# Optimization experiments

Measured on AMD Instinct MI355X. Metric: run time of the kernel, lower is better.

The kernel has to match this reference:

```python
import jax, jax.numpy as jnp
import numpy as np
import math

B, N, C = 8, 4096, 768
H = 12
DH = C // H
M = 256
LN_EPS = 1e-5


def setup_inputs() -> dict:
    key = jax.random.key(0)
    ks = jax.random.split(key, 7)
    x = jax.random.normal(ks[0], (B, N, C), dtype=jnp.float32)
    # torch Linear weight [out,in]; store transposed for y = x @ W
    W_qkv = jax.random.normal(ks[1], (C, 3 * C), dtype=jnp.float32) * (1.0 / math.sqrt(C))
    W_proj = jax.random.normal(ks[2], (C, C), dtype=jnp.float32) * (1.0 / math.sqrt(C))
    b_proj = jnp.zeros((C,), dtype=jnp.float32)
    gamma = jnp.ones((C,), dtype=jnp.float32)
    beta = jnp.zeros((C,), dtype=jnp.float32)
    random_features = jax.random.normal(ks[3], (M, DH), dtype=jnp.float32) / math.sqrt(DH)
    return {"x": x, "W_qkv": W_qkv, "W_proj": W_proj, "b_proj": b_proj,
            "gamma": gamma, "beta": beta, "random_features": random_features}


def _phi(t, random_features):
    # t: [B, H, N, DH] -> [B, H, N, M]; phi(x) = exp(w·x - ||x||^2/2) / sqrt(M)
    norm_sq = 0.5 * jnp.sum(t * t, axis=-1, keepdims=True)
    proj = jnp.einsum('bhnd,md->bhnm', t, random_features)
    return jnp.exp(proj - norm_sq) * (1.0 / math.sqrt(M))


def reference(x, W_qkv, W_proj, b_proj, gamma, beta, random_features):
    b, n, c = x.shape
    qkv = (x @ W_qkv).reshape(b, n, 3, H, DH)
    qkv = jnp.transpose(qkv, (2, 0, 3, 1, 4))  # [3, B, H, N, DH]
    q, k, v = qkv[0], qkv[1], qkv[2]

    q_p = _phi(q, random_features)  # [B,H,N,M]
    k_p = _phi(k, random_features)  # [B,H,N,M]

    kv = jnp.einsum('bhnm,bhnd->bhmd', k_p, v)       # [B,H,M,DH]
    out = jnp.einsum('bhnm,bhmd->bhnd', q_p, kv)     # [B,H,N,DH]

    k_sum = jnp.sum(k_p, axis=2)                      # [B,H,M]
    normalizer = jnp.einsum('bhnm,bhm->bhn', q_p, k_sum)[..., None]
    out = out / (normalizer + 1e-6)

    x_attn = jnp.transpose(out, (0, 2, 1, 3)).reshape(b, n, c)
    x_attn = x_attn @ W_proj + b_proj
    # dropout is identity in eval / p=0

    y = x + x_attn
    mu = jnp.mean(y, axis=-1, keepdims=True)
    var = jnp.mean(jnp.square(y - mu), axis=-1, keepdims=True)
    return (y - mu) * jax.lax.rsqrt(var + LN_EPS) * gamma + beta
```

## Files before the change

### kernel.cpp

```cpp
#include <hip/hip_runtime.h>
#include <hip/hip_fp16.h>


#define LOG2E 1.44269504088896340736f

typedef _Float16 half8 __attribute__((ext_vector_type(8)));
typedef _Float16 half4_t __attribute__((ext_vector_type(4)));
typedef _Float16 half2_t __attribute__((ext_vector_type(2)));
typedef float f32x4 __attribute__((ext_vector_type(4)));

#if __has_builtin(__builtin_amdgcn_fdot2)
#define FDOT2(a, b, c) __builtin_amdgcn_fdot2((a), (b), (c), false)
#else
#define FDOT2(a, b, c) \
  ((float)(a)[0] * (float)(b)[0] + ((float)(a)[1] * (float)(b)[1] + (c)))
#endif

static __device__ __forceinline__ half2_t pk2(float a, float b) {
#if __has_builtin(__builtin_amdgcn_cvt_pkrtz)
  return __builtin_bit_cast(half2_t, __builtin_amdgcn_cvt_pkrtz(a, b));
#else
  half2_t r; r[0] = (_Float16)a; r[1] = (_Float16)b; return r;
#endif
}

__device__ __forceinline__ void glds16(const _Float16* g, _Float16* s) {
  __builtin_amdgcn_global_load_lds(
      (const __attribute__((address_space(1))) void*)g,
      (__attribute__((address_space(3))) unsigned int*)s,
      16, 0, 0);
}


__global__ __launch_bounds__(256)
void prep(const float* __restrict__ x, const float* __restrict__ Wqkv,
          const float* __restrict__ Wproj, const float* __restrict__ rfm,
          _Float16* __restrict__ x_h, _Float16* __restrict__ wqkvT,
          _Float16* __restrict__ wprojT, _Float16* __restrict__ rfh) {
  __shared__ _Float16 T[64][72];
  const int bid = blockIdx.x;
  if (bid < 24576) {
    long i = ((long)bid * 256 + threadIdx.x) * 4;
    float4 v = *(const float4*)(x + i);
    half4_t h;
    h[0] = (_Float16)v.x; h[1] = (_Float16)v.y; h[2] = (_Float16)v.z; h[3] = (_Float16)v.w;
    *(half4_t*)(x_h + i) = h;
    return;
  }
  int tb = bid - 24576;
  if (tb < 576) {
    const float* src; _Float16* dst; int Csrc, r0, c0;
    if (tb < 432) {
      r0 = (tb / 36) * 64; c0 = (tb % 36) * 64; src = Wqkv; dst = wqkvT; Csrc = 2304;
    } else {
      int t2 = tb - 432;
      r0 = (t2 / 12) * 64; c0 = (t2 % 12) * 64; src = Wproj; dst = wprojT; Csrc = 768;
    }
    const int ri = threadIdx.x >> 4;
    const int ci = (threadIdx.x & 15) * 4;
#pragma unroll
    for (int rr = 0; rr < 4; ++rr) {
      float4 v = *(const float4*)(src + (long)(r0 + ri * 4 + rr) * Csrc + c0 + ci);
      T[ci + 0][ri * 4 + rr] = (_Float16)v.x;
      T[ci + 1][ri * 4 + rr] = (_Float16)v.y;
      T[ci + 2][ri * 4 + rr] = (_Float16)v.z;
      T[ci + 3][ri * 4 + rr] = (_Float16)v.w;
    }
    __syncthreads();
    const int wi = threadIdx.x >> 3;
    const int wj = (threadIdx.x & 7) * 8;
#pragma unroll
    for (int ww = 0; ww < 2; ++ww) {
      const int row = wi * 2 + ww;
      half8 h = *(const half8*)(&T[row][wj]);
      *(half8*)(dst + (long)(c0 + row) * 768 + r0 + wj) = h;
    }
  } else {
    int idx = (tb - 576) * 256 + threadIdx.x;
    if (idx < 16384) rfh[idx] = (_Float16)rfm[idx];
  }
}


__device__ __forceinline__ void stage_unit(const _Float16* __restrict__ G, int grow0,
                                           int kcol, _Float16* lds, int w, int l) {
#pragma unroll
  for (int j = 0; j < 2; ++j) {
    const int ci = w + j * 8;
    const int row = ci * 8 + (l >> 3);
    const int col8 = (l & 7) ^ (row & 7);
    glds16(G + (long)(grow0 + row) * 768 + kcol + col8 * 8, lds + ci * 512);
  }
}

static __device__ __forceinline__ half8 ldsw(const _Float16* buf, int r, int sl) {
  return *(const half8*)(buf + r * 64 + ((sl ^ (r & 7)) << 3));
}

__global__ __launch_bounds__(512)
void gemm_qkv(const _Float16* __restrict__ W, const _Float16* __restrict__ X,
              _Float16* __restrict__ qh, _Float16* __restrict__ kh,
              _Float16* __restrict__ vT,
              float* __restrict__ nsqLq, float* __restrict__ nsqLk) {
  __shared__ __align__(16) _Float16 As[32768];
  __shared__ __align__(16) _Float16 Bs[32768];
  const int tid = threadIdx.x;
  const int w = tid >> 6, l = tid & 63;
  const int lr = l & 15, kg = l >> 4;
  const int wr = w >> 2, wc = w & 3;

  const int bid = blockIdx.x;
  const int wg = (bid & 7) * 144 + (bid >> 3);
  const int m0 = (wg % 9) * 256;
  const int n0 = (wg / 9) * 256;

  stage_unit(W, m0,       0,  As,         w, l);
  stage_unit(X, n0,       0,  Bs,         w, l);
  stage_unit(X, n0 + 128, 0,  Bs + 8192,  w, l);
  stage_unit(W, m0 + 128, 0,  As + 8192,  w, l);
  stage_unit(W, m0,       64, As + 16384, w, l);
  stage_unit(X, n0,       64, Bs + 16384, w, l);
  stage_unit(X, n0 + 128, 64, Bs + 24576, w, l);
  asm volatile("s_waitcnt vmcnt(6)" ::: "memory");
  __builtin_amdgcn_s_barrier();

  f32x4 acc[8][4];
#pragma unroll
  for (int t = 0; t < 8; ++t)
#pragma unroll
    for (int u = 0; u < 4; ++u) acc[t][u] = (f32x4){0.f, 0.f, 0.f, 0.f};

  half8 a0[4][2], a1[4][2], b0[2][2], b1[2][2], b0n[2][2];
#pragma unroll
  for (int i = 0; i < 4; ++i) {
    const int r = wr * 16 + i * 32 + lr;
    a0[i][0] = ldsw(As, r, kg);
    a0[i][1] = ldsw(As, r, 4 + kg);
  }
#pragma unroll
  for (int j = 0; j < 2; ++j) {
    const int r = wc * 16 + j * 64 + lr;
    b0[j][0] = ldsw(Bs, r, kg);
    b0[j][1] = ldsw(Bs, r, 4 + kg);
  }

  for (int kt = 0; kt < 12; ++kt) {
    const int c = kt & 1, o = c ^ 1;
    const _Float16* Ac = As + c * 16384;
    const _Float16* Bc = Bs + c * 16384;
    const _Float16* An = As + o * 16384;
    const _Float16* Bn = Bs + o * 16384;

#pragma unroll
    for (int j = 0; j < 2; ++j) {
      const int r = 128 + wc * 16 + j * 64 + lr;
      b1[j][0] = ldsw(Bc, r, kg);
      b1[j][1] = ldsw(Bc, r, 4 + kg);
    }
    if (kt + 1 < 12)
      stage_unit(W, m0 + 128, (kt + 1) * 64, As + o * 16384 + 8192, w, l);
    __builtin_amdgcn_s_barrier();
    __builtin_amdgcn_s_setprio(1);
#pragma unroll
    for (int ks = 0; ks < 2; ++ks)
#pragma unroll
      for (int i = 0; i < 4; ++i)
#pragma unroll
        for (int j = 0; j < 2; ++j)
          acc[i][j] = __builtin_amdgcn_mfma_f32_16x16x32_f16(a0[i][ks], b0[j][ks],
                                                             acc[i][j], 0, 0, 0);
    __builtin_amdgcn_s_setprio(0);
    __builtin_amdgcn_s_barrier();

#pragma unroll
    for (int i = 0; i < 4; ++i) {
      const int r = 128 + wr * 16 + i * 32 + lr;
      a1[i][0] = ldsw(Ac, r, kg);
      a1[i][1] = ldsw(Ac, r, 4 + kg);
    }
    if (kt + 2 < 12)
      stage_unit(W, m0, (kt + 2) * 64, As + c * 16384, w, l);
    __builtin_amdgcn_s_barrier();
    __builtin_amdgcn_s_setprio(1);
#pragma unroll
    for (int ks = 0; ks < 2; ++ks)
#pragma unroll
      for (int i = 0; i < 4; ++i)
#pragma unroll
        for (int j = 0; j < 2; ++j)
          acc[i][2 + j] = __builtin_amdgcn_mfma_f32_16x16x32_f16(a0[i][ks], b1[j][ks],
                                                                 acc[i][2 + j], 0, 0, 0);
    __builtin_amdgcn_s_setprio(0);
    __builtin_amdgcn_s_barrier();

    if (kt + 2 < 12)
      stage_unit(X, n0, (kt + 2) * 64, Bs + c * 16384, w, l);
    __builtin_amdgcn_s_barrier();
    __builtin_amdgcn_s_setprio(1);
#pragma unroll
    for (int ks = 0; ks < 2; ++ks)
#pragma unroll
      for (int i = 0; i < 4; ++i)
#pragma unroll
        for (int j = 0; j < 2; ++j)
          acc[4 + i][2 + j] = __builtin_amdgcn_mfma_f32_16x16x32_f16(a1[i][ks], b1[j][ks],
                                                                     acc[4 + i][2 + j], 0, 0, 0);
    __builtin_amdgcn_s_setprio(0);
    __builtin_amdgcn_s_barrier();

    if (kt + 2 < 12)
      stage_unit(X, n0 + 128, (kt + 2) * 64, Bs + c * 16384 + 8192, w, l);
    if (kt < 10)
      asm volatile("s_waitcnt vmcnt(6)" ::: "memory");
    else
      asm volatile("s_waitcnt vmcnt(0)" ::: "memory");
    if (kt + 1 < 12) {
#pragma unroll
      for (int i = 0; i < 4; ++i) {
        const int r = wr * 16 + i * 32 + lr;
        a0[i][0] = ldsw(An, r, kg);
        a0[i][1] = ldsw(An, r, 4 + kg);
      }
#pragma unroll
      for (int j = 0; j < 2; ++j) {
        const int r = wc * 16 + j * 64 + lr;
        b0n[j][0] = ldsw(Bn, r, kg);
        b0n[j][1] = ldsw(Bn, r, 4 + kg);
      }
    }
    __builtin_amdgcn_s_barrier();
    __builtin_amdgcn_s_setprio(1);
#pragma unroll
    for (int ks = 0; ks < 2; ++ks)
#pragma unroll
      for (int i = 0; i < 4; ++i)
#pragma unroll
        for (int j = 0; j < 2; ++j)
          acc[4 + i][j] = __builtin_amdgcn_mfma_f32_16x16x32_f16(a1[i][ks], b0[j][ks],
                                                                 acc[4 + i][j], 0, 0, 0);
    __builtin_amdgcn_s_setprio(0);
    __builtin_amdgcn_s_barrier();
    if (kt + 1 < 12) {
#pragma unroll
      for (int j = 0; j < 2; ++j) { b0[j][0] = b0n[j][0]; b0[j][1] = b0n[j][1]; }
    }
  }

  const int which = (m0 >= 1536) ? 2 : ((m0 >= 768) ? 1 : 0);
  const int hbase = (m0 - which * 768) >> 6;
  const int b_ = n0 >> 12;
  const int nb = n0 & 4095;

  if (which < 2) {
    _Float16* dst = which ? kh : qh;
    float* nd = which ? nsqLk : nsqLq;
    float ns[4][4];
#pragma unroll
    for (int a = 0; a < 4; ++a)
#pragma unroll
      for (int b2 = 0; b2 < 4; ++b2) ns[a][b2] = 0.f;
#pragma unroll
    for (int t = 0; t < 8; ++t) {
      const int h = hbase + (t >> 1);
      const int d0 = wr * 16 + (t & 1) * 32 + kg * 4;
#pragma unroll
      for (int u = 0; u < 4; ++u) {
        const int n_ = nb + wc * 16 + u * 64 + lr;
        half2_t h01 = pk2(acc[t][u][0], acc[t][u][1]);
        half2_t h23 = pk2(acc[t][u][2], acc[t][u][3]);
        half4_t p4; p4[0] = h01[0]; p4[1] = h01[1]; p4[2] = h23[0]; p4[3] = h23[1];
        *(half4_t*)(dst + ((long)(b_ * 12 + h) * 4096 + n_) * 64 + d0) = p4;
#pragma unroll
        for (int r = 0; r < 4; ++r) { float f = (float)p4[r]; ns[t >> 1][u] += f * f; }
      }
    }
    float* nsP = (float*)As;
#pragma unroll
    for (int h2 = 0; h2 < 4; ++h2)
#pragma unroll
      for (int u = 0; u < 4; ++u) {
        float s = ns[h2][u];
        s += __shfl_xor(s, 16);
        s += __shfl_xor(s, 32);
        if (kg == 0) nsP[wr * 1024 + h2 * 256 + wc * 16 + u * 64 + lr] = s;
      }
    __syncthreads();
#pragma unroll
    for (int e = 0; e < 2; ++e) {
      const int idx = tid + e * 512;
      const int h2 = idx >> 8, tk = idx & 255;
      const float vsum = nsP[h2 * 256 + tk] + nsP[1024 + h2 * 256 + tk];
      nd[(long)(b_ * 12 + hbase + h2) * 4096 + nb + tk] = 0.5f * vsum * LOG2E + 4.0f;
    }
  } else {
#pragma unroll
    for (int t = 0; t < 8; ++t) {
      const int h = hbase + (t >> 1);
      const long hb = (long)(b_ * 12 + h) * 64;
      const int d0 = wr * 16 + (t & 1) * 32 + kg * 4;
#pragma unroll
      for (int u = 0; u < 4; ++u) {
        const int n_ = nb + wc * 16 + u * 64 + lr;
#pragma unroll
        for (int r = 0; r < 4; ++r)
          vT[(hb + d0 + r) * 4096 + n_] = (_Float16)acc[t][u][r];
      }
    }
  }
}


__global__ __launch_bounds__(256)
void gemm_proj(const _Float16* __restrict__ A, const _Float16* __restrict__ BT,
               float* __restrict__ Co, const float* __restrict__ bias,
               const float* __restrict__ resid) {
  __shared__ __align__(16) _Float16 As[128 * 32];
  __shared__ __align__(16) _Float16 Bs[128 * 32];
  const int tid = threadIdx.x;
  const int w = tid >> 6, l = tid & 63;
  const int lr = l & 15, kg = l >> 4;
  const int m0 = blockIdx.y * 128;
  const int n0 = blockIdx.x * 128;
  const int wm = (w >> 1) * 64, wn = (w & 1) * 64;

  const _Float16* gA = A + (long)(m0 + w * 32 + (l >> 2)) * 768 + (l & 3) * 8;
  const _Float16* gB = BT + (long)(n0 + w * 32 + (l >> 2)) * 768 + (l & 3) * 8;
  _Float16* sA = As + (w * 32) * 32;
  _Float16* sB = Bs + (w * 32) * 32;

  f32x4 acc[4][4];
#pragma unroll
  for (int t = 0; t < 4; ++t)
#pragma unroll
    for (int u = 0; u < 4; ++u) acc[t][u] = (f32x4){0.f, 0.f, 0.f, 0.f};

  for (int kc = 0; kc < 24; ++kc) {
    __syncthreads();
    glds16(gA, sA);
    glds16(gA + 16 * 768, sA + 16 * 32);
    glds16(gB, sB);
    glds16(gB + 16 * 768, sB + 16 * 32);
    gA += 32; gB += 32;
    __syncthreads();

    half8 af[4], bf[4];
#pragma unroll
    for (int t = 0; t < 4; ++t)
      af[t] = *(const half8*)(As + (wm + t * 16 + lr) * 32 + kg * 8);
#pragma unroll
    for (int u = 0; u < 4; ++u)
      bf[u] = *(const half8*)(Bs + (wn + u * 16 + lr) * 32 + kg * 8);
#pragma unroll
    for (int t = 0; t < 4; ++t)
#pragma unroll
      for (int u = 0; u < 4; ++u)
        acc[t][u] = __builtin_amdgcn_mfma_f32_16x16x32_f16(af[t], bf[u], acc[t][u], 0, 0, 0);
  }

#pragma unroll
  for (int u = 0; u < 4; ++u) {
    const int col = n0 + wn + u * 16 + lr;
    const float bv = bias[col];
#pragma unroll
    for (int t = 0; t < 4; ++t) {
      const int row = m0 + wm + t * 16 + kg * 4;
#pragma unroll
      for (int r = 0; r < 4; ++r) {
        long idx = (long)(row + r) * 768 + col;
        Co[idx] = acc[t][u][r] + bv + resid[idx];
      }
    }
  }
}


__global__ __launch_bounds__(256)
void kv_fused(const _Float16* __restrict__ kh, const _Float16* __restrict__ vT,
              const _Float16* __restrict__ rfh, const float* __restrict__ nsqLk,
              _Float16* __restrict__ kvpart, float* __restrict__ kspart) {
  __shared__ __align__(16) _Float16 Ka[64 * 32], Kb[64 * 32];
  __shared__ __align__(16) _Float16 Va[64 * 32], Vb[64 * 32];
  __shared__ __align__(16) _Float16 P[256 * 72];
  const int chunk = blockIdx.x, bh = blockIdx.y;
  const int tid = threadIdx.x, w = tid >> 6, l = tid & 63;
  const int lr = l & 15, kg = l >> 4;
  const long khbase = (long)bh * 4096 * 64;
  const long vtbase = (long)bh * 64 * 4096;
  const half2_t ONES = {(_Float16)1.f, (_Float16)1.f};

  half8 rf[4][2];
#pragma unroll
  for (int u = 0; u < 4; ++u)
#pragma unroll
    for (int ks = 0; ks < 2; ++ks)
      rf[u][ks] = *(const half8*)(rfh + (w * 64 + u * 16 + lr) * 64 + ks * 32 + kg * 8);

  f32x4 kvacc[4][4];
#pragma unroll
  for (int mt = 0; mt < 4; ++mt)
#pragma unroll
    for (int dt = 0; dt < 4; ++dt) kvacc[mt][dt] = (f32x4){0.f, 0.f, 0.f, 0.f};
  float ksacc[4] = {0.f, 0.f, 0.f, 0.f};

  for (int t8 = 0; t8 < 8; ++t8) {
    const int nt = chunk * 512 + t8 * 64;
    __syncthreads();
    if (w == 0) {
#pragma unroll
      for (int j = 0; j < 4; ++j)
        glds16(kh + khbase + (long)(nt + j * 16 + (l >> 2)) * 64 + (l & 3) * 8, Ka + j * 512);
    } else if (w == 1) {
#pragma unroll
      for (int j = 0; j < 4; ++j)
        glds16(kh + khbase + (long)(nt + j * 16 + (l >> 2)) * 64 + 32 + (l & 3) * 8, Kb + j * 512);
    } else if (w == 2) {
#pragma unroll
      for (int j = 0; j < 4; ++j)
        glds16(vT + vtbase + (long)(j * 16 + (l >> 2)) * 4096 + nt + (l & 3) * 8, Va + j * 512);
    } else {
#pragma unroll
      for (int j = 0; j < 4; ++j)
        glds16(vT + vtbase + (long)(j * 16 + (l >> 2)) * 4096 + nt + 32 + (l & 3) * 8, Vb + j * 512);
    }
    __syncthreads();

    half8 af[4][2];
#pragma unroll
    for (int tt = 0; tt < 4; ++tt) {
      af[tt][0] = *(const half8*)(Ka + (tt * 16 + lr) * 32 + kg * 8);
      af[tt][1] = *(const half8*)(Kb + (tt * 16 + lr) * 32 + kg * 8);
    }
    f32x4 sacc[4][4];
#pragma unroll
    for (int tt = 0; tt < 4; ++tt)
#pragma unroll
      for (int u = 0; u < 4; ++u) sacc[tt][u] = (f32x4){0.f, 0.f, 0.f, 0.f};
#pragma unroll
    for (int ks = 0; ks < 2; ++ks)
#pragma unroll
      for (int tt = 0; tt < 4; ++tt)
#pragma unroll
        for (int u = 0; u < 4; ++u)
          sacc[tt][u] = __builtin_amdgcn_mfma_f32_16x16x32_f16(af[tt][ks], rf[u][ks],
                                                               sacc[tt][u], 0, 0, 0);
    float4 nsq4[4];
#pragma unroll
    for (int tt = 0; tt < 4; ++tt)
      nsq4[tt] = *(const float4*)(nsqLk + (long)bh * 4096 + nt + tt * 16 + kg * 4);
#pragma unroll
    for (int tt = 0; tt < 4; ++tt)
#pragma unroll
      for (int u = 0; u < 4; ++u) {
        float e0 = exp2f(sacc[tt][u][0] * LOG2E - nsq4[tt].x);
        float e1 = exp2f(sacc[tt][u][1] * LOG2E - nsq4[tt].y);
        float e2 = exp2f(sacc[tt][u][2] * LOG2E - nsq4[tt].z);
        float e3 = exp2f(sacc[tt][u][3] * LOG2E - nsq4[tt].w);
        half2_t h01 = pk2(e0, e1), h23 = pk2(e2, e3);
        half4_t p4; p4[0] = h01[0]; p4[1] = h01[1]; p4[2] = h23[0]; p4[3] = h23[1];
        *(half4_t*)(P + (w * 64 + u * 16 + lr) * 72 + tt * 16 + kg * 4) = p4;
      }
#pragma unroll
    for (int ks = 0; ks < 2; ++ks) {
      half8 pa[4], bv[4];
#pragma unroll
      for (int mt = 0; mt < 4; ++mt)
        pa[mt] = *(const half8*)(P + (w * 64 + mt * 16 + lr) * 72 + ks * 32 + kg * 8);
#pragma unroll
      for (int dt = 0; dt < 4; ++dt)
        bv[dt] = *(const half8*)((ks == 0 ? Va : Vb) + (dt * 16 + lr) * 32 + kg * 8);
#pragma unroll
      for (int mt = 0; mt < 4; ++mt)
#pragma unroll
        for (int dt = 0; dt < 4; ++dt)
          kvacc[mt][dt] = __builtin_amdgcn_mfma_f32_16x16x32_f16(pa[mt], bv[dt],
                                                                 kvacc[mt][dt], 0, 0, 0);
#pragma unroll
      for (int mt = 0; mt < 4; ++mt) {
        const half2_t* pp = (const half2_t*)&pa[mt];
#pragma unroll
        for (int p = 0; p < 4; ++p) ksacc[mt] = FDOT2(pp[p], ONES, ksacc[mt]);
      }
    }
  }

#pragma unroll
  for (int mt = 0; mt < 4; ++mt) {
    float v = ksacc[mt];
    v += __shfl_xor(v, 16);
    v += __shfl_xor(v, 32);
    if (l < 16) kspart[((bh * 8 + chunk) << 8) + w * 64 + mt * 16 + l] = v;
  }
#pragma unroll
  for (int mt = 0; mt < 4; ++mt)
#pragma unroll
    for (int dt = 0; dt < 4; ++dt)
#pragma unroll
      for (int r = 0; r < 4; ++r)
        kvpart[(((long)(bh * 8 + chunk) * 256) + w * 64 + mt * 16 + kg * 4 + r) * 64 +
               dt * 16 + lr] = (_Float16)kvacc[mt][dt][r];
}


__global__ __launch_bounds__(256)
void reduce_all(const _Float16* __restrict__ kvpart, const float* __restrict__ kspart,
                _Float16* __restrict__ kvT, _Float16* __restrict__ ksumh) {
  if (blockIdx.x < 6144) {
    long i = (long)blockIdx.x * 256 + threadIdx.x;
    const int bh = (int)(i >> 14);
    const int rem = (int)(i & 16383);
    const int m = rem >> 6, d = rem & 63;
    float s = 0.f;
#pragma unroll
    for (int c = 0; c < 8; ++c)
      s += (float)kvpart[(((long)bh * 8 + c) * 256 + m) * 64 + d];
    kvT[(long)bh * 16384 + d * 256 + m] = (_Float16)s;
  } else {
    int i = (blockIdx.x - 6144) * 256 + threadIdx.x;
    int bh = i >> 8, m = i & 255;
    float s = 0.f;
#pragma unroll
    for (int c = 0; c < 8; ++c) s += kspart[((bh * 8 + c) << 8) + m];
    ksumh[i] = (_Float16)s;
  }
}


__global__ __launch_bounds__(256)
void attn_fused(const _Float16* __restrict__ qh, const _Float16* __restrict__ rfh,
                const float* __restrict__ nsqLq, const _Float16* __restrict__ kvT,
                const _Float16* __restrict__ ksumh, _Float16* __restrict__ attn) {
  __shared__ __align__(16) _Float16 Qa[64 * 32], Qb[64 * 32];
  __shared__ __align__(16) _Float16 KV[64 * 264];
  __shared__ __align__(16) _Float16 KS[256];
  __shared__ __align__(16) _Float16 P[64 * 264];
  __shared__ __align__(16) float NS[64];
  const int chunk = blockIdx.x, bh = blockIdx.y;
  const int b = bh / 12, h = bh % 12;
  const int tid = threadIdx.x, w = tid >> 6, l = tid & 63;
  const int lr = l & 15, kg = l >> 4;

  {
    const int d = tid >> 2, mb = (tid & 3) * 64;
#pragma unroll
    for (int j = 0; j < 8; ++j)
      *(half8*)(KV + d * 264 + mb + j * 8) =
          *(const half8*)(kvT + (long)bh * 16384 + d * 256 + mb + j * 8);
    if (tid < 32) *(half8*)(KS + tid * 8) = *(const half8*)(ksumh + bh * 256 + tid * 8);
  }

  half8 rf[4][2];
#pragma unroll
  for (int mt = 0; mt < 4; ++mt)
#pragma unroll
    for (int ks = 0; ks < 2; ++ks)
      rf[mt][ks] = *(const half8*)(rfh + (w * 64 + mt * 16 + lr) * 64 + ks * 32 + kg * 8);

  for (int t8 = 0; t8 < 4; ++t8) {
    const int nt = chunk * 256 + t8 * 64;
    __syncthreads();
    if (w == 0) {
#pragma unroll
      for (int j = 0; j < 4; ++j)
        glds16(qh + ((long)bh * 4096 + nt + j * 16 + (l >> 2)) * 64 + (l & 3) * 8, Qa + j * 512);
    } else if (w == 1) {
#pragma unroll
      for (int j = 0; j < 4; ++j)
        glds16(qh + ((long)bh * 4096 + nt + j * 16 + (l >> 2)) * 64 + 32 + (l & 3) * 8, Qb + j * 512);
    }
    __syncthreads();

    half8 bq[4][2];
#pragma unroll
    for (int tt = 0; tt < 4; ++tt) {
      bq[tt][0] = *(const half8*)(Qa + (tt * 16 + lr) * 32 + kg * 8);
      bq[tt][1] = *(const half8*)(Qb + (tt * 16 + lr) * 32 + kg * 8);
    }
    f32x4 sacc[4][4];
#pragma unroll
    for (int mt = 0; mt < 4; ++mt)
#pragma unroll
      for (int tt = 0; tt < 4; ++tt) sacc[mt][tt] = (f32x4){0.f, 0.f, 0.f, 0.f};
#pragma unroll
    for (int ks = 0; ks < 2; ++ks)
#pragma unroll
      for (int mt = 0; mt < 4; ++mt)
#pragma unroll
        for (int tt = 0; tt < 4; ++tt)
          sacc[mt][tt] = __builtin_amdgcn_mfma_f32_16x16x32_f16(rf[mt][ks], bq[tt][ks],
                                                                sacc[mt][tt], 0, 0, 0);
    float nsqv[4];
#pragma unroll
    for (int tt = 0; tt < 4; ++tt)
      nsqv[tt] = nsqLq[(long)bh * 4096 + nt + tt * 16 + lr];
#pragma unroll
    for (int mt = 0; mt < 4; ++mt)
#pragma unroll
      for (int tt = 0; tt < 4; ++tt) {
        float e0 = exp2f(sacc[mt][tt][0] * LOG2E - nsqv[tt]);
        float e1 = exp2f(sacc[mt][tt][1] * LOG2E - nsqv[tt]);
        float e2 = exp2f(sacc[mt][tt][2] * LOG2E - nsqv[tt]);
        float e3 = exp2f(sacc[mt][tt][3] * LOG2E - nsqv[tt]);
        half2_t h01 = pk2(e0, e1), h23 = pk2(e2, e3);
        half4_t p4; p4[0] = h01[0]; p4[1] = h01[1]; p4[2] = h23[0]; p4[3] = h23[1];
        *(half4_t*)(P + (tt * 16 + lr) * 264 + w * 64 + mt * 16 + kg * 4) = p4;
      }
    __syncthreads();

    f32x4 oacc[4];
#pragma unroll
    for (int u = 0; u < 4; ++u) oacc[u] = (f32x4){0.f, 0.f, 0.f, 0.f};
    float nacc = 0.f;
#pragma unroll
    for (int ks = 0; ks < 8; ++ks) {
      half8 ap = *(const half8*)(P + (w * 16 + lr) * 264 + ks * 32 + kg * 8);
      half8 kv8 = *(const half8*)(KS + ks * 32 + kg * 8);
      const half2_t* a2 = (const half2_t*)&ap;
      const half2_t* k2 = (const half2_t*)&kv8;
#pragma unroll
      for (int p = 0; p < 4; ++p) nacc = FDOT2(a2[p], k2[p], nacc);
#pragma unroll
      for (int u = 0; u < 4; ++u) {
        half8 bkv = *(const half8*)(KV + (u * 16 + lr) * 264 + ks * 32 + kg * 8);
        oacc[u] = __builtin_amdgcn_mfma_f32_16x16x32_f16(ap, bkv, oacc[u], 0, 0, 0);
      }
    }
    nacc += __shfl_xor(nacc, 16);
    nacc += __shfl_xor(nacc, 32);
    if (l < 16) NS[w * 16 + l] = nacc;
    f32x4 n4 = *(const f32x4*)(NS + w * 16 + kg * 4);
    float inv[4];
#pragma unroll
    for (int r = 0; r < 4; ++r) inv[r] = 1.f / (n4[r] + 1e-6f);
#pragma unroll
    for (int u = 0; u < 4; ++u)
#pragma unroll
      for (int r = 0; r < 4; ++r)
        attn[((long)b * 4096 + nt + w * 16 + kg * 4 + r) * 768 + h * 64 + u * 16 + lr] =
            (_Float16)(oacc[u][r] * inv[r]);
  }
}


__global__ __launch_bounds__(256)
void ln_kernel(const float* __restrict__ y, const float* __restrict__ gamma,
               const float* __restrict__ beta, float* __restrict__ outp) {
  const int wv = threadIdx.x >> 6, l = threadIdx.x & 63;
  const long row = (long)blockIdx.x * 4 + wv;
  const float* yr = y + row * 768;
  float v[12];
  float s = 0.f;
#pragma unroll
  for (int j = 0; j < 12; ++j) { v[j] = yr[l + j * 64]; s += v[j]; }
#pragma unroll
  for (int off = 32; off; off >>= 1) s += __shfl_xor(s, off);
  const float mu = s * (1.f / 768.f);
  float vs = 0.f;
#pragma unroll
  for (int j = 0; j < 12; ++j) { float d = v[j] - mu; vs += d * d; }
#pragma unroll
  for (int off = 32; off; off >>= 1) vs += __shfl_xor(vs, off);
  const float rstd = rsqrtf(vs * (1.f / 768.f) + 1e-5f);
  float* orp = outp + row * 768;
#pragma unroll
  for (int j = 0; j < 12; ++j)
    orp[l + j * 64] = (v[j] - mu) * rstd * gamma[l + j * 64] + beta[l + j * 64];
}


extern "C" void kernel_launch(void* const* d_in, const int* in_sizes, int n_in,
                              void* d_out, int out_size, void* d_ws, size_t ws_size,
                              hipStream_t stream) {
  const float* x = (const float*)d_in[0];
  const float* Wqkv = (const float*)d_in[1];
  const float* Wproj = (const float*)d_in[2];
  const float* bproj = (const float*)d_in[3];
  const float* gamma = (const float*)d_in[4];
  const float* beta = (const float*)d_in[5];
  const float* rfm = (const float*)d_in[6];

  char* ws = (char*)d_ws;
  size_t off = 0;
  auto alloc = [&](size_t bytes) -> void* {
    void* p = ws + off;
    off += (bytes + 255) & ~(size_t)255;
    return p;
  };
  char* regionA = (char*)alloc(50331648ULL);
  _Float16* x_h = (_Float16*)regionA;
  _Float16* kvpart = (_Float16*)regionA;
  _Float16* attn = (_Float16*)regionA;

  _Float16* wqkvT = (_Float16*)alloc(1769472ULL * 2);
  _Float16* wprojT = (_Float16*)alloc(589824ULL * 2);
  _Float16* rfh = (_Float16*)alloc(16384ULL * 2);
  _Float16* qh = (_Float16*)alloc(25165824ULL * 2);
  _Float16* kh = (_Float16*)alloc(25165824ULL * 2);
  _Float16* vT = (_Float16*)alloc(25165824ULL * 2);
  float* nsqLq = (float*)alloc(393216ULL * 4);
  float* nsqLk = (float*)alloc(393216ULL * 4);
  float* kspart = (float*)alloc(96ULL * 8 * 256 * 4);
  _Float16* kvT = (_Float16*)alloc(96ULL * 16384 * 2);
  _Float16* ksumh = (_Float16*)alloc(96ULL * 256 * 2);

  float* y = (float*)d_out;

  prep<<<25216, 256, 0, stream>>>(x, Wqkv, Wproj, rfm, x_h, wqkvT, wprojT, rfh);
  gemm_qkv<<<1152, 512, 0, stream>>>(wqkvT, x_h, qh, kh, vT, nsqLq, nsqLk);
  kv_fused<<<dim3(8, 96), 256, 0, stream>>>(kh, vT, rfh, nsqLk, kvpart, kspart);
  reduce_all<<<6240, 256, 0, stream>>>(kvpart, kspart, kvT, ksumh);
  attn_fused<<<dim3(16, 96), 256, 0, stream>>>(qh, rfh, nsqLq, kvT, ksumh, attn);
  gemm_proj<<<dim3(6, 256), 256, 0, stream>>>(attn, wprojT, y, bproj, x);
  ln_kernel<<<8192, 256, 0, stream>>>(y, gamma, beta, y);
}
```

Before: 648.4 us.

## Register-prefetch next K/V/Q tiles and restructure GEMM fragment reloads

In the kv and q-feature kernels, the wave-specialised global-to-LDS copies are replaced with per-thread register staging. Each thread prefetches the next 64-row tile into registers while the current tile is computed, then writes it to LDS after a barrier. This removes one barrier per iteration and hides global latency behind the MFMA and exp work. The QKV GEMM main loop also drops the cross-iteration prefetch of A/B fragments from the other buffer and reloads them from the current buffer inside each phase. That lowers register pressure but exposes some LDS latency at the start of each iteration.

Result: faster. 622.7 us (-4.0%).

```diff
diff --git a/kernel.cpp b/kernel.cpp
--- a/kernel.cpp
+++ b/kernel.cpp
@@ -130,32 +130,23 @@
 #pragma unroll
     for (int u = 0; u < 4; ++u) acc[t][u] = (f32x4){0.f, 0.f, 0.f, 0.f};
 
-  half8 a0[4][2], a1[4][2], b0[2][2], b1[2][2], b0n[2][2];
-#pragma unroll
-  for (int i = 0; i < 4; ++i) {
-    const int r = wr * 16 + i * 32 + lr;
-    a0[i][0] = ldsw(As, r, kg);
-    a0[i][1] = ldsw(As, r, 4 + kg);
-  }
-#pragma unroll
-  for (int j = 0; j < 2; ++j) {
-    const int r = wc * 16 + j * 64 + lr;
-    b0[j][0] = ldsw(Bs, r, kg);
-    b0[j][1] = ldsw(Bs, r, 4 + kg);
-  }
-
   for (int kt = 0; kt < 12; ++kt) {
     const int c = kt & 1, o = c ^ 1;
     const _Float16* Ac = As + c * 16384;
     const _Float16* Bc = Bs + c * 16384;
-    const _Float16* An = As + o * 16384;
-    const _Float16* Bn = Bs + o * 16384;
-
+    half8 aR[4][2], bR0[2][2], bR1[2][2];
+
+#pragma unroll
+    for (int i = 0; i < 4; ++i) {
+      const int r = wr * 16 + i * 32 + lr;
+      aR[i][0] = ldsw(Ac, r, kg);
+      aR[i][1] = ldsw(Ac, r, 4 + kg);
+    }
 #pragma unroll
     for (int j = 0; j < 2; ++j) {
-      const int r = 128 + wc * 16 + j * 64 + lr;
-      b1[j][0] = ldsw(Bc, r, kg);
-      b1[j][1] = ldsw(Bc, r, 4 + kg);
+      const int r = wc * 16 + j * 64 + lr;
+      bR0[j][0] = ldsw(Bc, r, kg);
+      bR0[j][1] = ldsw(Bc, r, 4 + kg);
     }
     if (kt + 1 < 12)
       stage_unit(W, m0 + 128, (kt + 1) * 64, As + o * 16384 + 8192, w, l);
@@ -167,16 +158,16 @@
       for (int i = 0; i < 4; ++i)
 #pragma unroll
         for (int j = 0; j < 2; ++j)
-          acc[i][j] = __builtin_amdgcn_mfma_f32_16x16x32_f16(a0[i][ks], b0[j][ks],
+          acc[i][j] = __builtin_amdgcn_mfma_f32_16x16x32_f16(aR[i][ks], bR0[j][ks],
                                                              acc[i][j], 0, 0, 0);
     __builtin_amdgcn_s_setprio(0);
     __builtin_amdgcn_s_barrier();
 
 #pragma unroll
-    for (int i = 0; i < 4; ++i) {
-      const int r = 128 + wr * 16 + i * 32 + lr;
-      a1[i][0] = ldsw(Ac, r, kg);
-      a1[i][1] = ldsw(Ac, r, 4 + kg);
+    for (int j = 0; j < 2; ++j) {
+      const int r = 128 + wc * 16 + j * 64 + lr;
+      bR1[j][0] = ldsw(Bc, r, kg);
+      bR1[j][1] = ldsw(Bc, r, 4 + kg);
     }
     if (kt + 2 < 12)
       stage_unit(W, m0, (kt + 2) * 64, As + c * 16384, w, l);
@@ -188,11 +179,17 @@
       for (int i = 0; i < 4; ++i)
 #pragma unroll
         for (int j = 0; j < 2; ++j)
-          acc[i][2 + j] = __builtin_amdgcn_mfma_f32_16x16x32_f16(a0[i][ks], b1[j][ks],
+          acc[i][2 + j] = __builtin_amdgcn_mfma_f32_16x16x32_f16(aR[i][ks], bR1[j][ks],
                                                                  acc[i][2 + j], 0, 0, 0);
     __builtin_amdgcn_s_setprio(0);
     __builtin_amdgcn_s_barrier();
 
+#pragma unroll
+    for (int i = 0; i < 4; ++i) {
+      const int r = 128 + wr * 16 + i * 32 + lr;
+      aR[i][0] = ldsw(Ac, r, kg);
+      aR[i][1] = ldsw(Ac, r, 4 + kg);
+    }
     if (kt + 2 < 12)
       stage_unit(X, n0, (kt + 2) * 64, Bs + c * 16384, w, l);
     __builtin_amdgcn_s_barrier();
@@ -203,7 +200,7 @@
       for (int i = 0; i < 4; ++i)
 #pragma unroll
         for (int j = 0; j < 2; ++j)
-          acc[4 + i][2 + j] = __builtin_amdgcn_mfma_f32_16x16x32_f16(a1[i][ks], b1[j][ks],
+          acc[4 + i][2 + j] = __builtin_amdgcn_mfma_f32_16x16x32_f16(aR[i][ks], bR1[j][ks],
                                                                      acc[4 + i][2 + j], 0, 0, 0);
     __builtin_amdgcn_s_setprio(0);
     __builtin_amdgcn_s_barrier();
@@ -214,20 +211,6 @@
       asm volatile("s_waitcnt vmcnt(6)" ::: "memory");
     else
       asm volatile("s_waitcnt vmcnt(0)" ::: "memory");
-    if (kt + 1 < 12) {
-#pragma unroll
-      for (int i = 0; i < 4; ++i) {
-        const int r = wr * 16 + i * 32 + lr;
-        a0[i][0] = ldsw(An, r, kg);
-        a0[i][1] = ldsw(An, r, 4 + kg);
-      }
-#pragma unroll
-      for (int j = 0; j < 2; ++j) {
-        const int r = wc * 16 + j * 64 + lr;
-        b0n[j][0] = ldsw(Bn, r, kg);
-        b0n[j][1] = ldsw(Bn, r, 4 + kg);
-      }
-    }
     __builtin_amdgcn_s_barrier();
     __builtin_amdgcn_s_setprio(1);
 #pragma unroll
@@ -236,14 +219,10 @@
       for (int i = 0; i < 4; ++i)
 #pragma unroll
         for (int j = 0; j < 2; ++j)
-          acc[4 + i][j] = __builtin_amdgcn_mfma_f32_16x16x32_f16(a1[i][ks], b0[j][ks],
+          acc[4 + i][j] = __builtin_amdgcn_mfma_f32_16x16x32_f16(aR[i][ks], bR0[j][ks],
                                                                  acc[4 + i][j], 0, 0, 0);
     __builtin_amdgcn_s_setprio(0);
     __builtin_amdgcn_s_barrier();
-    if (kt + 1 < 12) {
-#pragma unroll
-      for (int j = 0; j < 2; ++j) { b0[j][0] = b0n[j][0]; b0[j][1] = b0n[j][1]; }
-    }
   }
 
   const int which = (m0 >= 1536) ? 2 : ((m0 >= 768) ? 1 : 0);
@@ -388,6 +367,23 @@
   const long vtbase = (long)bh * 64 * 4096;
   const half2_t ONES = {(_Float16)1.f, (_Float16)1.f};
 
+  const int srow = tid >> 2, scg = tid & 3;
+  _Float16* sKdst = ((scg < 2) ? Ka : Kb) + srow * 32 + (scg & 1) * 16;
+  _Float16* sVdst = ((scg < 2) ? Va : Vb) + srow * 32 + (scg & 1) * 16;
+  const _Float16* gK = kh + khbase + (long)srow * 64 + scg * 16;
+  const _Float16* gV = vT + vtbase + (long)srow * 4096 + scg * 16;
+
+  half8 stK0, stK1, stV0, stV1;
+  {
+    const long nt0 = (long)chunk * 512;
+    stK0 = *(const half8*)(gK + nt0 * 64);
+    stK1 = *(const half8*)(gK + nt0 * 64 + 8);
+    stV0 = *(const half8*)(gV + nt0);
+    stV1 = *(const half8*)(gV + nt0 + 8);
+    *(half8*)(sKdst) = stK0; *(half8*)(sKdst + 8) = stK1;
+    *(half8*)(sVdst) = stV0; *(half8*)(sVdst + 8) = stV1;
+  }
+
   half8 rf[4][2];
 #pragma unroll
   for (int u = 0; u < 4; ++u)
@@ -405,24 +401,14 @@
   for (int t8 = 0; t8 < 8; ++t8) {
     const int nt = chunk * 512 + t8 * 64;
     __syncthreads();
-    if (w == 0) {
-#pragma unroll
-      for (int j = 0; j < 4; ++j)
-        glds16(kh + khbase + (long)(nt + j * 16 + (l >> 2)) * 64 + (l & 3) * 8, Ka + j * 512);
-    } else if (w == 1) {
-#pragma unroll
-      for (int j = 0; j < 4; ++j)
-        glds16(kh + khbase + (long)(nt + j * 16 + (l >> 2)) * 64 + 32 + (l & 3) * 8, Kb + j * 512);
-    } else if (w == 2) {
-#pragma unroll
-      for (int j = 0; j < 4; ++j)
-        glds16(vT + vtbase + (long)(j * 16 + (l >> 2)) * 4096 + nt + (l & 3) * 8, Va + j * 512);
-    } else {
-#pragma unroll
-      for (int j = 0; j < 4; ++j)
-        glds16(vT + vtbase + (long)(j * 16 + (l >> 2)) * 4096 + nt + 32 + (l & 3) * 8, Vb + j * 512);
-    }
-    __syncthreads();
+
+    if (t8 + 1 < 8) {
+      const long ntn = nt + 64;
+      stK0 = *(const half8*)(gK + ntn * 64);
+      stK1 = *(const half8*)(gK + ntn * 64 + 8);
+      stV0 = *(const half8*)(gV + ntn);
+      stV1 = *(const half8*)(gV + ntn + 8);
+    }
 
     half8 af[4][2];
 #pragma unroll
@@ -480,6 +466,12 @@
 #pragma unroll
         for (int p = 0; p < 4; ++p) ksacc[mt] = FDOT2(pp[p], ONES, ksacc[mt]);
       }
+    }
+
+    __syncthreads();
+    if (t8 + 1 < 8) {
+      *(half8*)(sKdst) = stK0; *(half8*)(sKdst + 8) = stK1;
+      *(half8*)(sVdst) = stV0; *(half8*)(sVdst + 8) = stV1;
     }
   }
 
@@ -539,6 +531,18 @@
   const int tid = threadIdx.x, w = tid >> 6, l = tid & 63;
   const int lr = l & 15, kg = l >> 4;
 
+  const int srow = tid >> 2, scg = tid & 3;
+  _Float16* sQdst = ((scg < 2) ? Qa : Qb) + srow * 32 + (scg & 1) * 16;
+  const _Float16* gQ = qh + ((long)bh * 4096 + srow) * 64 + scg * 16;
+
+  half8 sq0, sq1;
+  {
+    const long nt0 = (long)chunk * 256;
+    sq0 = *(const half8*)(gQ + nt0 * 64);
+    sq1 = *(const half8*)(gQ + nt0 * 64 + 8);
+    *(half8*)(sQdst) = sq0; *(half8*)(sQdst + 8) = sq1;
+  }
+
   {
     const int d = tid >> 2, mb = (tid & 3) * 64;
 #pragma unroll
@@ -558,16 +562,6 @@
   for (int t8 = 0; t8 < 4; ++t8) {
     const int nt = chunk * 256 + t8 * 64;
     __syncthreads();
-    if (w == 0) {
-#pragma unroll
-      for (int j = 0; j < 4; ++j)
-        glds16(qh + ((long)bh * 4096 + nt + j * 16 + (l >> 2)) * 64 + (l & 3) * 8, Qa + j * 512);
-    } else if (w == 1) {
-#pragma unroll
-      for (int j = 0; j < 4; ++j)
-        glds16(qh + ((long)bh * 4096 + nt + j * 16 + (l >> 2)) * 64 + 32 + (l & 3) * 8, Qb + j * 512);
-    }
-    __syncthreads();
 
     half8 bq[4][2];
 #pragma unroll
@@ -575,6 +569,12 @@
       bq[tt][0] = *(const half8*)(Qa + (tt * 16 + lr) * 32 + kg * 8);
       bq[tt][1] = *(const half8*)(Qb + (tt * 16 + lr) * 32 + kg * 8);
     }
+    if (t8 + 1 < 4) {
+      const long ntn = nt + 64;
+      sq0 = *(const half8*)(gQ + ntn * 64);
+      sq1 = *(const half8*)(gQ + ntn * 64 + 8);
+    }
+
     f32x4 sacc[4][4];
 #pragma unroll
     for (int mt = 0; mt < 4; ++mt)
@@ -605,6 +605,9 @@
         *(half4_t*)(P + (tt * 16 + lr) * 264 + w * 64 + mt * 16 + kg * 4) = p4;
       }
     __syncthreads();
+    if (t8 + 1 < 4) {
+      *(half8*)(sQdst) = sq0; *(half8*)(sQdst + 8) = sq1;
+    }
 
     f32x4 oacc[4];
 #pragma unroll
```
